# Kernel tuning notes

Measured on AMD Instinct MI355X. Metric: run time of the kernel, lower is better.

## Reference

```python
import jax, jax.numpy as jnp
import numpy as np

NUM_EMBEDDINGS = 8192
EMBEDDING_DIM = 512
COMMITMENT_COST = 0.25
EMA_DECAY = 0.99
EPS = 1e-5


def setup_inputs() -> dict:
    key = jax.random.key(0)
    k1, k2, k3, k4 = jax.random.split(key, 4)
    B = 32768
    z = jax.random.normal(k1, (B, EMBEDDING_DIM), dtype=jnp.float32)
    weight = jax.random.normal(k2, (NUM_EMBEDDINGS, EMBEDDING_DIM), dtype=jnp.float32)
    ema_cluster_size = jax.random.uniform(k3, (NUM_EMBEDDINGS,), dtype=jnp.float32)
    ema_dw = jax.random.normal(k4, (NUM_EMBEDDINGS, EMBEDDING_DIM), dtype=jnp.float32)
    return {"z": z, "weight": weight, "ema_cluster_size": ema_cluster_size, "ema_dw": ema_dw}


def reference(z, weight, ema_cluster_size, ema_dw):
    K = weight.shape[0]
    # Squared-L2 distances: (B, K) = |z|^2 + |e|^2 - 2 z e^T
    distances = (
        jnp.sum(z * z, axis=1, keepdims=True)
        + jnp.sum(weight * weight, axis=1)
        - 2.0 * (z @ weight.T)
    )
    indices = jnp.argmin(distances, axis=1)          # (B,)
    quantized_raw = weight[indices]                  # (B, D) gather

    # EMA codebook update (training-mode buffers; one-hot scatter-add == segment_sum)
    counts = jax.ops.segment_sum(jnp.ones(z.shape[0], dtype=z.dtype), indices, num_segments=K)
    dw = jax.ops.segment_sum(z, indices, num_segments=K)  # encodings.T @ z
    new_cluster_size = ema_cluster_size * EMA_DECAY + (1.0 - EMA_DECAY) * counts
    new_ema_dw = ema_dw * EMA_DECAY + (1.0 - EMA_DECAY) * dw
    n = jnp.sum(new_cluster_size)
    cluster_size = (new_cluster_size + EPS) / (n + K * EPS) * n
    new_weight = new_ema_dw / cluster_size[:, None]

    commitment_loss = COMMITMENT_COST * jnp.mean((z - jax.lax.stop_gradient(quantized_raw)) ** 2)
    quantized = z + jax.lax.stop_gradient(quantized_raw - z)  # straight-through
    return quantized, indices, commitment_loss, new_weight, new_cluster_size, new_ema_dw
```

## Files before the change

kernel.cpp:

```cpp
#include <hip/hip_runtime.h>

#define B_N 32768
#define D_N 512
#define K_N 8192
#define EMA 0.99f
#define ONE_M_EMA 0.01f
#define EPS_ 1e-5f
#define CCOST 0.25f

#define ZP_OFF 295936ull
#define WP_OFF 67404800ull
#define WS_NEED (WP_OFF + 16777216ull)
#define CNT_OFF    295936ull
#define OFFS_OFF   332800ull
#define CURS_OFF   365568ull
#define ROWL_OFF   398336ull
#define LPART_OFF  529408ull

typedef __attribute__((ext_vector_type(8))) short bf16x8;
typedef __attribute__((ext_vector_type(4))) float f32x4;

__global__ __launch_bounds__(256) void prep_kernel(const float* __restrict__ w,
                                                   const float* __restrict__ ecs,
                                                   float* __restrict__ wsq,
                                                   float* __restrict__ ncs_out) {
  int row  = blockIdx.x * 4 + (threadIdx.x >> 6);
  int lane = threadIdx.x & 63;
  const float* p = w + (size_t)row * D_N + lane * 8;
  float4 a = *(const float4*)p;
  float4 b = *(const float4*)(p + 4);
  float s = a.x*a.x + a.y*a.y + a.z*a.z + a.w*a.w
          + b.x*b.x + b.y*b.y + b.z*b.z + b.w*b.w;
  #pragma unroll
  for (int off = 32; off; off >>= 1) s += __shfl_down(s, off);
  if (lane == 0) wsq[row] = s;

  int gid = blockIdx.x * 256 + threadIdx.x;
  if (gid < K_N) ncs_out[gid] = EMA * ecs[gid];
}

__global__ __launch_bounds__(256) void prep_nedw(const float4* __restrict__ edw,
                                                 float4* __restrict__ nedw) {
  int i = blockIdx.x * 256 + threadIdx.x;
  float4 v = edw[i];
  v.x *= EMA; v.y *= EMA; v.z *= EMA; v.w *= EMA;
  nedw[i] = v;
}

__global__ __launch_bounds__(256) void split_z(const float* __restrict__ x,
                                               ushort* __restrict__ xp) {
  int g   = blockIdx.x * 256 + threadIdx.x;
  int row = g >> 6, c = g & 63;
  const float* src = x + (size_t)row * 512 + c * 8;
  float v[8];
  *(float4*)&v[0] = *(const float4*)&src[0];
  *(float4*)&v[4] = *(const float4*)&src[4];
  uint hw[4], lw[4];
  #pragma unroll
  for (int i = 0; i < 4; i++) {
    uint b0 = __float_as_uint(v[2*i]);
    uint b1 = __float_as_uint(v[2*i+1]);
    float r0 = v[2*i]   - __uint_as_float(b0 & 0xFFFF0000u);
    float r1 = v[2*i+1] - __uint_as_float(b1 & 0xFFFF0000u);
    hw[i] = (b0 >> 16) | (b1 & 0xFFFF0000u);
    lw[i] = (__float_as_uint(r0) >> 16) | (__float_as_uint(r1) & 0xFFFF0000u);
  }
  int si  = c >> 2;
  int p   = (c & 3) ^ ((row >> 1) & 3);
  size_t sstr = (size_t)B_N * 32;
  size_t base = (size_t)row * 32 + (size_t)p * 8;
  *(uint4*)&xp[(size_t)si * sstr + base]        = (uint4){hw[0], hw[1], hw[2], hw[3]};
  *(uint4*)&xp[(size_t)(16 + si) * sstr + base] = (uint4){lw[0], lw[1], lw[2], lw[3]};
}

__global__ __launch_bounds__(256) void split_w(const float* __restrict__ x,
                                               ushort* __restrict__ xp,
                                               float* __restrict__ wsq) {
  int g   = blockIdx.x * 256 + threadIdx.x;
  int row = g >> 6, c = g & 63;
  const float* src = x + (size_t)row * 512 + c * 8;
  float v[8];
  *(float4*)&v[0] = *(const float4*)&src[0];
  *(float4*)&v[4] = *(const float4*)&src[4];
  uint hw[4], lw[4]; float w2 = 0.f;
  #pragma unroll
  for (int i = 0; i < 4; i++) {
    uint b0 = __float_as_uint(v[2*i]);
    uint b1 = __float_as_uint(v[2*i+1]);
    float r0 = v[2*i]   - __uint_as_float(b0 & 0xFFFF0000u);
    float r1 = v[2*i+1] - __uint_as_float(b1 & 0xFFFF0000u);
    hw[i] = (b0 >> 16) | (b1 & 0xFFFF0000u);
    lw[i] = (__float_as_uint(r0) >> 16) | (__float_as_uint(r1) & 0xFFFF0000u);
    w2 += v[2*i]*v[2*i] + v[2*i+1]*v[2*i+1];
  }
  int si  = c >> 2;
  int p   = (c & 3) ^ ((row >> 1) & 3);
  size_t sstr = (size_t)K_N * 32;
  size_t base = (size_t)row * 32 + (size_t)p * 8;
  *(uint4*)&xp[(size_t)si * sstr + base]        = (uint4){hw[0], hw[1], hw[2], hw[3]};
  *(uint4*)&xp[(size_t)(16 + si) * sstr + base] = (uint4){lw[0], lw[1], lw[2], lw[3]};
  #pragma unroll
  for (int off = 32; off; off >>= 1) w2 += __shfl_down(w2, off);
  if (c == 0) wsq[row] = w2;
}

constexpr int COLT2 = 8;

#define GLDS(SRC, DST) __builtin_amdgcn_global_load_lds((const unsigned int*)(SRC), (unsigned int*)(DST), 16, 0, 0)

#define STAGE1(S, SL)                                                          \
  {                                                                            \
    const int s__ = (S);                                                       \
    const int zsl_ = (s__ < 32) ? (s__ & 15) : (s__ - 16);     \
    const int wsl_ = (s__ < 32) ? s__ : (s__ - 32);            \
    GLDS(zA + (size_t)zsl_ * 2097152,        (char*)As[SL] + t * 16);          \
    GLDS(zA + (size_t)zsl_ * 2097152 + 8192, (char*)As[SL] + 8192 + t * 16);   \
    const size_t wOfs_ = (size_t)wsl_ * 524288 + (size_t)ctf * 16384;          \
    GLDS(wB + wOfs_,        (char*)Bs[SL] + t * 16);                           \
    GLDS(wB + wOfs_ + 8192, (char*)Bs[SL] + 8192 + t * 16);                    \
  }

#define LOADFRAG(AX, BX, G)                                                    \
  {                                                                            \
    const char* Ab_ = (const char*)As[(G) & 3] + aoff;                         \
    const char* Bb_ = (const char*)Bs[(G) & 3] + boff;                         \
    _Pragma("unroll")                                                          \
    for (int i_ = 0; i_ < 8; i_++) AX[i_] = *(const bf16x8*)(Ab_ + i_ * 1024); \
    _Pragma("unroll")                                                          \
    for (int j_ = 0; j_ < 4; j_++) BX[j_] = *(const bf16x8*)(Bb_ + j_ * 1024); \
  }

#define MFMABLK(AX, BX)                                                        \
  {                                                                            \
    __builtin_amdgcn_s_setprio(1);                                             \
    _Pragma("unroll")                                                          \
    for (int i_ = 0; i_ < 8; i_++)                                             \
      _Pragma("unroll")                                                        \
      for (int j_ = 0; j_ < 4; j_++)                                           \
        acc[i_][j_] = __builtin_amdgcn_mfma_f32_16x16x32_bf16(AX[i_], BX[j_],  \
                                                        acc[i_][j_], 0, 0, 0); \
    __builtin_amdgcn_s_setprio(0);                                             \
  }

#define PHASE2(G2)                                                             \
  {                                                                            \
    const int g2_ = (G2);                                                      \
    if (g2_ + 4 <= 383) {                         \
      STAGE1(sf,     sf & 3)                                                   \
      STAGE1(sf + 1, (sf + 1) & 3)                                             \
      sf += 2; if (sf == 48) { sf = 0; ctf++; }                                \
    }                                                                          \
    MFMABLK(aE, bE)                                              \
    if (g2_ + 2 <= 383) LOADFRAG(aE, bE, g2_ + 2)    \
    MFMABLK(aO, bO)                                            \
    if (g2_ + 3 <= 383) LOADFRAG(aO, bO, g2_ + 3)                              \
    asm volatile("s_waitcnt lgkmcnt(0)" ::: "memory");                         \
    asm volatile("s_waitcnt vmcnt(0)" ::: "memory");                           \
    __builtin_amdgcn_s_barrier();                                              \
    __builtin_amdgcn_sched_barrier(0);                                         \
  }

__global__ __launch_bounds__(512, 2) void score3r(
    const ushort* __restrict__ zp, const ushort* __restrict__ wp,
    const float* __restrict__ wsq, unsigned long long* __restrict__ packed) {
  __shared__ ushort As[4][8192];
  __shared__ ushort Bs[4][8192];
  __shared__ float wsqs[2048];
  __shared__ unsigned long long best2[256][4];

  const int t = threadIdx.x, lane = t & 63, wid = t >> 6;
  const int wm = wid >> 2, wn = wid & 3;
  const int l15 = lane & 15, lg = (lane >> 4) & 3;
  const int row0 = blockIdx.x * 256;
  const int cg0  = blockIdx.y * 2048;

  const char* zA = (const char*)zp + ((size_t)(row0 + (t >> 2)) * 64 + (size_t)(t & 3) * 16);
  const char* wB = (const char*)wp + ((size_t)(cg0  + (t >> 2)) * 64 + (size_t)(t & 3) * 16);

  const int swz  = (l15 >> 1) & 3;
  const int aoff = (wm * 128 + l15) * 64 + ((lg ^ swz) * 16);
  const int boff = (wn * 64  + l15) * 64 + ((lg ^ swz) * 16);

  { float4 v = *(const float4*)&wsq[cg0 + t * 4]; *(float4*)&wsqs[t * 4] = v; }
  if (t < 256) { best2[t][0] = ~0ull; best2[t][1] = ~0ull; best2[t][2] = ~0ull; best2[t][3] = ~0ull; }
  __syncthreads();

  int sf = 4, ctf = 0;

  #pragma unroll
  for (int s0 = 0; s0 < 4; s0++) {
    GLDS(zA + (size_t)s0 * 2097152,        (char*)As[s0] + t * 16);
    GLDS(zA + (size_t)s0 * 2097152 + 8192, (char*)As[s0] + 8192 + t * 16);
    GLDS(wB + (size_t)s0 * 524288,         (char*)Bs[s0] + t * 16);
    GLDS(wB + (size_t)s0 * 524288 + 8192,  (char*)Bs[s0] + 8192 + t * 16);
  }
  asm volatile("s_waitcnt vmcnt(0)" ::: "memory");
  __builtin_amdgcn_s_barrier();
  __builtin_amdgcn_sched_barrier(0);

  bf16x8 aE[8], bE[4], aO[8], bO[4];
  LOADFRAG(aE, bE, 0)
  LOADFRAG(aO, bO, 1)
  asm volatile("s_waitcnt lgkmcnt(0)" ::: "memory");
  __builtin_amdgcn_s_barrier();
  __builtin_amdgcn_sched_barrier(0);

  for (int ct = 0; ct < COLT2; ct++) {
    f32x4 acc[8][4];
    #pragma unroll
    for (int i = 0; i < 8; i++)
      #pragma unroll
      for (int j = 0; j < 4; j++) acc[i][j] = (f32x4){0.f, 0.f, 0.f, 0.f};

    for (int p = 0; p < 24; p++) {
      PHASE2(ct * 48 + 2 * p)
    }

    float rv[32]; int rx[32];
    #pragma unroll
    for (int i = 0; i < 8; i++)
      #pragma unroll
      for (int r = 0; r < 4; r++) {
        float bvv = 3.4e38f; int bii = 0;
        #pragma unroll
        for (int j = 0; j < 4; j++) {
          float wq = wsqs[ct * 256 + wn * 64 + j * 16 + l15];
          float dist = wq - 2.0f * acc[i][j][r];
          int c = cg0 + ct * 256 + wn * 64 + j * 16 + l15;
          if (dist < bvv) { bvv = dist; bii = c; }
        }
        rv[i * 4 + r] = bvv; rx[i * 4 + r] = bii;
      }
    #pragma unroll
    for (int e = 0; e < 32; e++) {
      float v = rv[e]; int ix = rx[e];
      #pragma unroll
      for (int m = 1; m < 16; m <<= 1) {
        float ov = __shfl_xor(v, m, 64);
        int   oi = __shfl_xor(ix, m, 64);
        if (ov < v || (ov == v && oi < ix)) { v = ov; ix = oi; }
      }
      rv[e] = v; rx[e] = ix;
    }
    #pragma unroll
    for (int half = 0; half < 2; half++) {
      const int e0 = l15 + half * 16;
      float bvv = 0.f; int bii = 0;
      #pragma unroll
      for (int e = 0; e < 32; e++) {
        bool p2 = (e == e0);
        bvv = p2 ? rv[e] : bvv; bii = p2 ? rx[e] : bii;
      }
      unsigned u = __float_as_uint(bvv);
      u = (u & 0x80000000u) ? ~u : (u | 0x80000000u);
      unsigned long long key = ((unsigned long long)u << 32) | (unsigned)bii;
      const int rowl = wm * 128 + (e0 >> 2) * 16 + lg * 4 + (e0 & 3);
      unsigned long long cur = best2[rowl][wn];
      if (key < cur) best2[rowl][wn] = key;
    }
  }

  __syncthreads();
  if (t < 256) {
    unsigned long long k0 = best2[t][0], k1 = best2[t][1];
    unsigned long long k2 = best2[t][2], k3 = best2[t][3];
    unsigned long long m0 = k0 < k1 ? k0 : k1;
    unsigned long long m1 = k2 < k3 ? k2 : k3;
    atomicMin(&packed[row0 + t], m0 < m1 ? m0 : m1);
  }
}

constexpr int LDP = 40;
constexpr int KSPLIT = 8, COLT = K_N / KSPLIT / 128;
__device__ __forceinline__ void stage16(const float* __restrict__ g,
                                        ushort* __restrict__ h,
                                        ushort* __restrict__ l) {
  float v[16];
  *(float4*)&v[0]  = *(const float4*)&g[0];
  *(float4*)&v[4]  = *(const float4*)&g[4];
  *(float4*)&v[8]  = *(const float4*)&g[8];
  *(float4*)&v[12] = *(const float4*)&g[12];
  uint hw[8], lw[8];
  #pragma unroll
  for (int i = 0; i < 8; i++) {
    uint b0 = __float_as_uint(v[2*i]);
    uint b1 = __float_as_uint(v[2*i+1]);
    float r0 = v[2*i]   - __uint_as_float(b0 & 0xFFFF0000u);
    float r1 = v[2*i+1] - __uint_as_float(b1 & 0xFFFF0000u);
    hw[i] = (b0 >> 16) | (b1 & 0xFFFF0000u);
    lw[i] = (__float_as_uint(r0) >> 16) | (__float_as_uint(r1) & 0xFFFF0000u);
  }
  ((uint4*)h)[0] = *(uint4*)&hw[0];
  ((uint4*)h)[1] = *(uint4*)&hw[4];
  ((uint4*)l)[0] = *(uint4*)&lw[0];
  ((uint4*)l)[1] = *(uint4*)&lw[4];
}

__global__ __launch_bounds__(256, 2) void score_argmin_mfma(
    const float* __restrict__ z, const float* __restrict__ w,
    const float* __restrict__ wsq, unsigned long long* __restrict__ packed) {
  __shared__ ushort Ah[128][LDP];
  __shared__ ushort Al[128][LDP];
  __shared__ ushort Bh[128][LDP];
  __shared__ ushort Bl[128][LDP];
  const int t = threadIdx.x, lane = t & 63, wid = t >> 6;
  const int wm = wid >> 1, wn = wid & 1;
  const int l15 = lane & 15, lg = lane >> 4;
  const int row0 = blockIdx.x * 128;
  const int ks0  = blockIdx.y * (K_N / KSPLIT);
  const int srow = t >> 1, skq = (t & 1) * 16;
  float rmin[16]; int ridx[16];
  #pragma unroll
  for (int e = 0; e < 16; e++) { rmin[e] = 3.4e38f; ridx[e] = 0; }
  for (int ct = 0; ct < COLT; ct++) {
    const int c0 = ks0 + ct * 128;
    f32x4 acc[4][4];
    #pragma unroll
    for (int i = 0; i < 4; i++)
      #pragma unroll
      for (int j = 0; j < 4; j++) acc[i][j] = (f32x4){0.f, 0.f, 0.f, 0.f};
    for (int k0 = 0; k0 < D_N; k0 += 32) {
      __syncthreads();
      stage16(&z[(size_t)(row0 + srow) * D_N + k0 + skq], &Ah[srow][skq], &Al[srow][skq]);
      stage16(&w[(size_t)(c0   + srow) * D_N + k0 + skq], &Bh[srow][skq], &Bl[srow][skq]);
      __syncthreads();
      bf16x8 ah[4], al[4], bh[4], bl[4];
      #pragma unroll
      for (int i = 0; i < 4; i++) {
        ah[i] = *(const bf16x8*)&Ah[wm*64 + i*16 + l15][lg*8];
        al[i] = *(const bf16x8*)&Al[wm*64 + i*16 + l15][lg*8];
        bh[i] = *(const bf16x8*)&Bh[wn*64 + i*16 + l15][lg*8];
        bl[i] = *(const bf16x8*)&Bl[wn*64 + i*16 + l15][lg*8];
      }
      #pragma unroll
      for (int i = 0; i < 4; i++)
        #pragma unroll
        for (int j = 0; j < 4; j++) {
          acc[i][j] = __builtin_amdgcn_mfma_f32_16x16x32_bf16(ah[i], bh[j], acc[i][j], 0, 0, 0);
          acc[i][j] = __builtin_amdgcn_mfma_f32_16x16x32_bf16(ah[i], bl[j], acc[i][j], 0, 0, 0);
          acc[i][j] = __builtin_amdgcn_mfma_f32_16x16x32_bf16(al[i], bh[j], acc[i][j], 0, 0, 0);
        }
    }
    float wq[4];
    #pragma unroll
    for (int j = 0; j < 4; j++) wq[j] = wsq[c0 + wn*64 + j*16 + l15];
    #pragma unroll
    for (int i = 0; i < 4; i++)
      #pragma unroll
      for (int r = 0; r < 4; r++) {
        const int e = i * 4 + r;
        #pragma unroll
        for (int j = 0; j < 4; j++) {
          float dist = wq[j] - 2.0f * acc[i][j][r];
          if (dist < rmin[e]) { rmin[e] = dist; ridx[e] = c0 + wn*64 + j*16 + l15; }
        }
      }
  }
  #pragma unroll
  for (int e = 0; e < 16; e++) {
    float v = rmin[e]; int ix = ridx[e];
    #pragma unroll
    for (int m = 1; m < 16; m <<= 1) {
      float ov = __shfl_xor(v, m, 64);
      int   oi = __shfl_xor(ix, m, 64);
      if (ov < v || (ov == v && oi < ix)) { v = ov; ix = oi; }
    }
    rmin[e] = v; ridx[e] = ix;
  }
  const int s = l15;
  float bv = 0.f; int bi = 0;
  #pragma unroll
  for (int e = 0; e < 16; e++) {
    bool p = (e == s);
    bv = p ? rmin[e] : bv;
    bi = p ? ridx[e] : bi;
  }
  unsigned u = __float_as_uint(bv);
  u = (u & 0x80000000u) ? ~u : (u | 0x80000000u);
  unsigned long long key = ((unsigned long long)u << 32) | (unsigned)bi;
  atomicMin(&packed[row0 + wm*64 + (s >> 2)*16 + lg*4 + (s & 3)], key);
}

__global__ __launch_bounds__(256) void count_kernel(
    const unsigned long long* __restrict__ packed, int* __restrict__ cnt,
    float* __restrict__ idxout) {
  int row = blockIdx.x * 256 + threadIdx.x;
  int idx = (int)(packed[row] & 0xFFFFFFFFull);
  idxout[row] = (float)idx;
  atomicAdd(&cnt[idx], 1);
}

__global__ __launch_bounds__(256) void scan_kernel(const int* __restrict__ cnt,
                                                   int* __restrict__ offs,
                                                   int* __restrict__ cursor) {
  int t = threadIdx.x;
  int base = t * 32;
  int local[32];
  int s = 0;
  #pragma unroll
  for (int i = 0; i < 32; i++) { local[i] = s; s += cnt[base + i]; }
  __shared__ int ps[257];
  ps[t + 1] = s;
  if (t == 0) ps[0] = 0;
  __syncthreads();
  if (t == 0) { for (int i = 1; i <= 256; i++) ps[i] += ps[i - 1]; }
  __syncthreads();
  int e = ps[t];
  #pragma unroll
  for (int i = 0; i < 32; i++) {
    int o = e + local[i];
    offs[base + i] = o; cursor[base + i] = o;
  }
  if (t == 255) offs[8192] = ps[256];
}

__global__ __launch_bounds__(256) void scatter_ids(
    const unsigned long long* __restrict__ packed, int* __restrict__ cursor,
    int* __restrict__ rowlist) {
  int row = blockIdx.x * 256 + threadIdx.x;
  int idx = (int)(packed[row] & 0xFFFFFFFFull);
  int pos = atomicAdd(&cursor[idx], 1);
  rowlist[pos] = row;
}

__global__ __launch_bounds__(256) void seg_accum(
    const float* __restrict__ z, const float* __restrict__ edw,
    const float* __restrict__ ecs, const int* __restrict__ offs,
    const int* __restrict__ rowlist, float* __restrict__ nedw_out,
    float* __restrict__ ncs_out) {
  int k = blockIdx.x, t = threadIdx.x;
  int s0 = offs[k], s1 = offs[k + 1];
  float ax = 0.f, ay = 0.f;
  for (int r = s0; r < s1; r++) {
    int row = rowlist[r];
    float2 zv = *(const float2*)&z[(size_t)row * D_N + t * 2];
    ax += zv.x; ay += zv.y;
  }
  float2 ev = *(const float2*)&edw[(size_t)k * D_N + t * 2];
  float2 o;
  o.x = EMA * ev.x + ONE_M_EMA * ax;
  o.y = EMA * ev.y + ONE_M_EMA * ay;
  *(float2*)&nedw_out[(size_t)k * D_N + t * 2] = o;
  if (t == 0) ncs_out[k] = EMA * ecs[k] + ONE_M_EMA * (float)(s1 - s0);
}

__global__ __launch_bounds__(256) void quant_loss(
    const float* __restrict__ z, const float* __restrict__ w,
    const unsigned long long* __restrict__ packed,
    float* __restrict__ qout, float* __restrict__ lpart) {
  int row = blockIdx.x, t = threadIdx.x;
  int idx = (int)(packed[row] & 0xFFFFFFFFull);
  float2 zv = *(const float2*)&z[(size_t)row * D_N + t * 2];
  float2 wv = *(const float2*)&w[(size_t)idx * D_N + t * 2];
  float2 q;
  q.x = zv.x + (wv.x - zv.x);
  q.y = zv.y + (wv.y - zv.y);
  *(float2*)&qout[(size_t)row * D_N + t * 2] = q;
  float dx = zv.x - wv.x, dy = zv.y - wv.y;
  float s = dx * dx + dy * dy;
  #pragma unroll
  for (int off = 32; off; off >>= 1) s += __shfl_down(s, off);
  __shared__ float part[4];
  if ((t & 63) == 0) part[t >> 6] = s;
  __syncthreads();
  if (t == 0) lpart[row] = part[0] + part[1] + part[2] + part[3];
}

__global__ __launch_bounds__(256) void reduce2(const float* __restrict__ ncs_out,
                                               const float* __restrict__ lpart,
                                               float* __restrict__ nsum,
                                               float* __restrict__ loss_sum) {
  int t = threadIdx.x;
  float s1 = 0.f, s2 = 0.f;
  for (int i = t; i < K_N; i += 256) s1 += ncs_out[i];
  for (int i = t; i < B_N; i += 256) s2 += lpart[i];
  #pragma unroll
  for (int off = 32; off; off >>= 1) {
    s1 += __shfl_down(s1, off);
    s2 += __shfl_down(s2, off);
  }
  __shared__ float p1[4], p2[4];
  if ((t & 63) == 0) { p1[t >> 6] = s1; p2[t >> 6] = s2; }
  __syncthreads();
  if (t == 0) {
    nsum[0]     = p1[0] + p1[1] + p1[2] + p1[3];
    loss_sum[0] = p2[0] + p2[1] + p2[2] + p2[3];
  }
}

__global__ __launch_bounds__(256) void gather_scatter(
    const float* __restrict__ z, const float* __restrict__ w,
    const unsigned long long* __restrict__ packed,
    float* __restrict__ qout, float* __restrict__ idxout,
    float* __restrict__ ncs_out, float* __restrict__ nedw_out,
    float* __restrict__ loss_sum) {
  int row = blockIdx.x;
  int t   = threadIdx.x;
  int idx = (int)(packed[row] & 0xFFFFFFFFull);
  float2 zv = *(const float2*)&z[(size_t)row * D_N + t * 2];
  float2 wv = *(const float2*)&w[(size_t)idx * D_N + t * 2];
  float2 q;
  q.x = zv.x + (wv.x - zv.x);
  q.y = zv.y + (wv.y - zv.y);
  *(float2*)&qout[(size_t)row * D_N + t * 2] = q;
  float dx = zv.x - wv.x, dy = zv.y - wv.y;
  float s = dx*dx + dy*dy;
  #pragma unroll
  for (int off = 32; off; off >>= 1) s += __shfl_down(s, off);
  __shared__ float part[4];
  if ((t & 63) == 0) part[t >> 6] = s;
  __syncthreads();
  if (t == 0) {
    atomicAdd(loss_sum, part[0] + part[1] + part[2] + part[3]);
    atomicAdd(&ncs_out[idx], ONE_M_EMA);
    idxout[row] = (float)idx;
  }
  atomicAdd(&nedw_out[(size_t)idx * D_N + t*2],     ONE_M_EMA * zv.x);
  atomicAdd(&nedw_out[(size_t)idx * D_N + t*2 + 1], ONE_M_EMA * zv.y);
}

__global__ __launch_bounds__(256) void reduce_n(const float* __restrict__ ncs_out,
                                                float* __restrict__ nsum) {
  int t = threadIdx.x;
  float s = 0.f;
  for (int i = t; i < K_N; i += 256) s += ncs_out[i];
  #pragma unroll
  for (int off = 32; off; off >>= 1) s += __shfl_down(s, off);
  __shared__ float part[4];
  if ((t & 63) == 0) part[t >> 6] = s;
  __syncthreads();
  if (t == 0) nsum[0] = part[0] + part[1] + part[2] + part[3];
}

__global__ __launch_bounds__(256) void finalize(
    const float* __restrict__ ncs_out, const float* __restrict__ nedw_out,
    float* __restrict__ nw_out, const float* __restrict__ nsum,
    const float* __restrict__ loss_sum, float* __restrict__ loss_out) {
  size_t i = (size_t)blockIdx.x * 256 + threadIdx.x;
  float n = nsum[0];
  int k = (int)(i >> 9);
  float nv = ncs_out[k];
  float cs = (nv + EPS_) / (n + K_N * EPS_) * n;
  nw_out[i] = nedw_out[i] / cs;
  if (i == 0) loss_out[0] = CCOST * loss_sum[0] / (float)((size_t)B_N * D_N);
}

extern "C" void kernel_launch(void* const* d_in, const int* in_sizes, int n_in,
                              void* d_out, int out_size, void* d_ws, size_t ws_size,
                              hipStream_t stream) {
  const float* z   = (const float*)d_in[0];
  const float* w   = (const float*)d_in[1];
  const float* ecs = (const float*)d_in[2];
  const float* edw = (const float*)d_in[3];

  float* out      = (float*)d_out;
  float* qout     = out;
  float* idxout   = out + (size_t)B_N * D_N;
  float* loss_out = idxout + B_N;
  float* nw_out   = loss_out + 1;
  float* ncs_out  = nw_out + (size_t)K_N * D_N;
  float* nedw_out = ncs_out + K_N;

  unsigned long long* packed = (unsigned long long*)d_ws;
  float* wsq      = (float*)((char*)d_ws + 262144);
  float* loss_sum = (float*)((char*)d_ws + 294912);
  float* nsum     = loss_sum + 1;

  hipMemsetAsync(d_ws, 0xFF, 262144, stream);
  hipMemsetAsync((void*)loss_sum, 0, 8, stream);

  if (ws_size >= WS_NEED) {
    ushort* zp  = (ushort*)((char*)d_ws + ZP_OFF);
    ushort* wp  = (ushort*)((char*)d_ws + WP_OFF);
    int* cnt    = (int*)((char*)d_ws + CNT_OFF);
    int* offs   = (int*)((char*)d_ws + OFFS_OFF);
    int* cursor = (int*)((char*)d_ws + CURS_OFF);
    int* rowl   = (int*)((char*)d_ws + ROWL_OFF);
    float* lpart= (float*)((char*)d_ws + LPART_OFF);

    split_z<<<8192, 256, 0, stream>>>(z, zp);
    split_w<<<2048, 256, 0, stream>>>(w, wp, wsq);
    score3r<<<dim3(128, 4), 512, 0, stream>>>(zp, wp, wsq, packed);
    hipMemsetAsync((void*)cnt, 0, K_N * sizeof(int), stream);
    count_kernel<<<B_N / 256, 256, 0, stream>>>(packed, cnt, idxout);
    scan_kernel<<<1, 256, 0, stream>>>(cnt, offs, cursor);
    scatter_ids<<<B_N / 256, 256, 0, stream>>>(packed, cursor, rowl);
    seg_accum<<<K_N, 256, 0, stream>>>(z, edw, ecs, offs, rowl, nedw_out, ncs_out);
    quant_loss<<<B_N, 256, 0, stream>>>(z, w, packed, qout, lpart);
    reduce2<<<1, 256, 0, stream>>>(ncs_out, lpart, nsum, loss_sum);
  } else {
    prep_kernel<<<2048, 256, 0, stream>>>(w, ecs, wsq, ncs_out);
    prep_nedw<<<4096, 256, 0, stream>>>((const float4*)edw, (float4*)nedw_out);
    score_argmin_mfma<<<dim3(B_N / 128, KSPLIT), 256, 0, stream>>>(z, w, wsq, packed);
    gather_scatter<<<B_N, 256, 0, stream>>>(z, w, packed, qout, idxout,
                                            ncs_out, nedw_out, loss_sum);
    reduce_n<<<1, 256, 0, stream>>>(ncs_out, nsum);
  }

  finalize<<<K_N * D_N / 256, 256, 0, stream>>>(ncs_out, nedw_out, nw_out,
                                                nsum, loss_sum, loss_out);
}
```

Measured before the change: 1.019 ms.

## Shrink score tile to 128 rows with 4 waves and double-buffered LDS

Replaces the 256-row, 8-wave scoring kernel with a 128-row, 4-wave version that uses two LDS stages instead of four and stages one k-slice per phase. Row-norm values are now read straight from global memory into registers rather than cached in LDS. The aim is to cut LDS footprint and per-block sync cost so more blocks fit per CU and the grid gets wider. In exchange, each W tile is reused across fewer z rows, which doubles codebook traffic, and the shallower prefetch may expose load latency.

```diff
diff --git a/kernel.cpp b/kernel.cpp
--- a/kernel.cpp
+++ b/kernel.cpp
@@ -108,29 +108,31 @@
 
 #define GLDS(SRC, DST) __builtin_amdgcn_global_load_lds((const unsigned int*)(SRC), (unsigned int*)(DST), 16, 0, 0)
 
-#define STAGE1(S, SL)                                                          \
+#define STAGE4(SS)                                                             \
   {                                                                            \
-    const int s__ = (S);                                                       \
-    const int zsl_ = (s__ < 32) ? (s__ & 15) : (s__ - 16);     \
-    const int wsl_ = (s__ < 32) ? s__ : (s__ - 32);            \
-    GLDS(zA + (size_t)zsl_ * 2097152,        (char*)As[SL] + t * 16);          \
-    GLDS(zA + (size_t)zsl_ * 2097152 + 8192, (char*)As[SL] + 8192 + t * 16);   \
+    const int zsl_ = (sf < 32) ? (sf & 15) : (sf - 16);        \
+    const int wsl_ = (sf < 32) ? sf : (sf - 32);               \
+    GLDS(zA + (size_t)zsl_ * 2097152,        (char*)As[SS] + t * 16);          \
+    GLDS(zA + (size_t)zsl_ * 2097152 + 4096, (char*)As[SS] + 4096 + t * 16);   \
     const size_t wOfs_ = (size_t)wsl_ * 524288 + (size_t)ctf * 16384;          \
-    GLDS(wB + wOfs_,        (char*)Bs[SL] + t * 16);                           \
-    GLDS(wB + wOfs_ + 8192, (char*)Bs[SL] + 8192 + t * 16);                    \
-  }
-
-#define LOADFRAG(AX, BX, G)                                                    \
+    GLDS(wB + wOfs_,         (char*)Bs[SS] + t * 16);                          \
+    GLDS(wB + wOfs_ + 4096,  (char*)Bs[SS] + 4096  + t * 16);                  \
+    GLDS(wB + wOfs_ + 8192,  (char*)Bs[SS] + 8192  + t * 16);                  \
+    GLDS(wB + wOfs_ + 12288, (char*)Bs[SS] + 12288 + t * 16);                  \
+    sf++; if (sf == 48) { sf = 0; ctf++; }                                     \
+  }
+
+#define LOADFRAG4(AX, BX, RS)                                                  \
   {                                                                            \
-    const char* Ab_ = (const char*)As[(G) & 3] + aoff;                         \
-    const char* Bb_ = (const char*)Bs[(G) & 3] + boff;                         \
+    const char* Ab_ = (const char*)As[RS] + aoff;                              \
+    const char* Bb_ = (const char*)Bs[RS] + boff;                              \
     _Pragma("unroll")                                                          \
     for (int i_ = 0; i_ < 8; i_++) AX[i_] = *(const bf16x8*)(Ab_ + i_ * 1024); \
     _Pragma("unroll")                                                          \
     for (int j_ = 0; j_ < 4; j_++) BX[j_] = *(const bf16x8*)(Bb_ + j_ * 1024); \
   }
 
-#define MFMABLK(AX, BX)                                                        \
+#define MFMABLK4(AX, BX)                                                       \
   {                                                                            \
     __builtin_amdgcn_s_setprio(1);                                             \
     _Pragma("unroll")                                                          \
@@ -142,65 +144,49 @@
     __builtin_amdgcn_s_setprio(0);                                             \
   }
 
-#define PHASE2(G2)                                                             \
+#define PH4(AC, BC, AL, BL, RS, SS, G)                                         \
   {                                                                            \
-    const int g2_ = (G2);                                                      \
-    if (g2_ + 4 <= 383) {                         \
-      STAGE1(sf,     sf & 3)                                                   \
-      STAGE1(sf + 1, (sf + 1) & 3)                                             \
-      sf += 2; if (sf == 48) { sf = 0; ctf++; }                                \
-    }                                                                          \
-    MFMABLK(aE, bE)                                              \
-    if (g2_ + 2 <= 383) LOADFRAG(aE, bE, g2_ + 2)    \
-    MFMABLK(aO, bO)                                            \
-    if (g2_ + 3 <= 383) LOADFRAG(aO, bO, g2_ + 3)                              \
+    const int g_ = (G);                                                        \
+    if (g_ + 1 <= 383) LOADFRAG4(AL, BL, RS)                                   \
+    if (g_ + 2 <= 383) STAGE4(SS)                                              \
+    MFMABLK4(AC, BC)                                                           \
     asm volatile("s_waitcnt lgkmcnt(0)" ::: "memory");                         \
-    asm volatile("s_waitcnt vmcnt(0)" ::: "memory");                           \
+    if (g_ <= 382) { asm volatile("s_waitcnt vmcnt(0)" ::: "memory"); }        \
     __builtin_amdgcn_s_barrier();                                              \
     __builtin_amdgcn_sched_barrier(0);                                         \
   }
 
-__global__ __launch_bounds__(512, 2) void score3r(
+__global__ __launch_bounds__(256, 2) void score4(
     const ushort* __restrict__ zp, const ushort* __restrict__ wp,
     const float* __restrict__ wsq, unsigned long long* __restrict__ packed) {
-  __shared__ ushort As[4][8192];
-  __shared__ ushort Bs[4][8192];
-  __shared__ float wsqs[2048];
-  __shared__ unsigned long long best2[256][4];
-
-  const int t = threadIdx.x, lane = t & 63, wid = t >> 6;
-  const int wm = wid >> 2, wn = wid & 3;
+  __shared__ ushort As[2][4096];
+  __shared__ ushort Bs[2][8192];
+  __shared__ unsigned long long best2[128][4];
+
+  const int t = threadIdx.x, lane = t & 63, wn = t >> 6;
   const int l15 = lane & 15, lg = (lane >> 4) & 3;
-  const int row0 = blockIdx.x * 256;
+  const int row0 = blockIdx.x * 128;
   const int cg0  = blockIdx.y * 2048;
 
   const char* zA = (const char*)zp + ((size_t)(row0 + (t >> 2)) * 64 + (size_t)(t & 3) * 16);
   const char* wB = (const char*)wp + ((size_t)(cg0  + (t >> 2)) * 64 + (size_t)(t & 3) * 16);
 
   const int swz  = (l15 >> 1) & 3;
-  const int aoff = (wm * 128 + l15) * 64 + ((lg ^ swz) * 16);
-  const int boff = (wn * 64  + l15) * 64 + ((lg ^ swz) * 16);
-
-  { float4 v = *(const float4*)&wsq[cg0 + t * 4]; *(float4*)&wsqs[t * 4] = v; }
-  if (t < 256) { best2[t][0] = ~0ull; best2[t][1] = ~0ull; best2[t][2] = ~0ull; best2[t][3] = ~0ull; }
-  __syncthreads();
-
-  int sf = 4, ctf = 0;
-
-  #pragma unroll
-  for (int s0 = 0; s0 < 4; s0++) {
-    GLDS(zA + (size_t)s0 * 2097152,        (char*)As[s0] + t * 16);
-    GLDS(zA + (size_t)s0 * 2097152 + 8192, (char*)As[s0] + 8192 + t * 16);
-    GLDS(wB + (size_t)s0 * 524288,         (char*)Bs[s0] + t * 16);
-    GLDS(wB + (size_t)s0 * 524288 + 8192,  (char*)Bs[s0] + 8192 + t * 16);
-  }
+  const int aoff = l15 * 64 + ((lg ^ swz) * 16);
+  const int boff = (wn * 64 + l15) * 64 + ((lg ^ swz) * 16);
+
+  if (t < 128) { best2[t][0] = ~0ull; best2[t][1] = ~0ull; best2[t][2] = ~0ull; best2[t][3] = ~0ull; }
+  __syncthreads();
+
+  int sf = 0, ctf = 0;
+  STAGE4(0)
+  STAGE4(1)
   asm volatile("s_waitcnt vmcnt(0)" ::: "memory");
   __builtin_amdgcn_s_barrier();
   __builtin_amdgcn_sched_barrier(0);
 
   bf16x8 aE[8], bE[4], aO[8], bO[4];
-  LOADFRAG(aE, bE, 0)
-  LOADFRAG(aO, bO, 1)
+  LOADFRAG4(aE, bE, 0)
   asm volatile("s_waitcnt lgkmcnt(0)" ::: "memory");
   __builtin_amdgcn_s_barrier();
   __builtin_amdgcn_sched_barrier(0);
@@ -213,9 +199,14 @@
       for (int j = 0; j < 4; j++) acc[i][j] = (f32x4){0.f, 0.f, 0.f, 0.f};
 
     for (int p = 0; p < 24; p++) {
-      PHASE2(ct * 48 + 2 * p)
+      const int g = ct * 48 + 2 * p;
+      PH4(aE, bE, aO, bO, 1, 0, g)
+      PH4(aO, bO, aE, bE, 0, 1, g + 1)
     }
 
+    float wq[4];
+    #pragma unroll
+    for (int j = 0; j < 4; j++) wq[j] = wsq[cg0 + ct * 256 + wn * 64 + j * 16 + l15];
     float rv[32]; int rx[32];
     #pragma unroll
     for (int i = 0; i < 8; i++)
@@ -224,8 +215,7 @@
         float bvv = 3.4e38f; int bii = 0;
         #pragma unroll
         for (int j = 0; j < 4; j++) {
-          float wq = wsqs[ct * 256 + wn * 64 + j * 16 + l15];
-          float dist = wq - 2.0f * acc[i][j][r];
+          float dist = wq[j] - 2.0f * acc[i][j][r];
           int c = cg0 + ct * 256 + wn * 64 + j * 16 + l15;
           if (dist < bvv) { bvv = dist; bii = c; }
         }
@@ -254,14 +244,14 @@
       unsigned u = __float_as_uint(bvv);
       u = (u & 0x80000000u) ? ~u : (u | 0x80000000u);
       unsigned long long key = ((unsigned long long)u << 32) | (unsigned)bii;
-      const int rowl = wm * 128 + (e0 >> 2) * 16 + lg * 4 + (e0 & 3);
+      const int rowl = (e0 >> 2) * 16 + lg * 4 + (e0 & 3);
       unsigned long long cur = best2[rowl][wn];
       if (key < cur) best2[rowl][wn] = key;
     }
   }
 
   __syncthreads();
-  if (t < 256) {
+  if (t < 128) {
     unsigned long long k0 = best2[t][0], k1 = best2[t][1];
     unsigned long long k2 = best2[t][2], k3 = best2[t][3];
     unsigned long long m0 = k0 < k1 ? k0 : k1;
@@ -580,7 +570,7 @@
 
     split_z<<<8192, 256, 0, stream>>>(z, zp);
     split_w<<<2048, 256, 0, stream>>>(w, wp, wsq);
-    score3r<<<dim3(128, 4), 512, 0, stream>>>(zp, wp, wsq, packed);
+    score4<<<dim3(B_N / 128, 4), 256, 0, stream>>>(zp, wp, wsq, packed);
     hipMemsetAsync((void*)cnt, 0, K_N * sizeof(int), stream);
     count_kernel<<<B_N / 256, 256, 0, stream>>>(packed, cnt, idxout);
     scan_kernel<<<1, 256, 0, stream>>>(cnt, offs, cursor);
```

After: 1.051 ms. 3.1% more time.
